# Kernel optimization log

Measured on AMD Instinct MI355X. Metric: run time of the kernel, lower is better.

Reference implementation:

```python
import jax, jax.numpy as jnp
import numpy as np

NEG_SLOPE = 0.01
H = 128  # hidden_conv_1 == hidden_conv_2


def leaky(x):
    return jnp.where(x >= 0, x, NEG_SLOPE * x)


def gru_cell(x, h, w_ih, w_hh, b_ih, b_hh):
    # PyTorch GRUCell: gates stacked [r, z, n] along dim 0 of w_ih/w_hh
    gi = x @ w_ih.T + b_ih  # [N, 3H]
    gh = h @ w_hh.T + b_hh
    ir, iz, inn = jnp.split(gi, 3, axis=-1)
    hr, hz, hn = jnp.split(gh, 3, axis=-1)
    r = jax.nn.sigmoid(ir + hr)
    z = jax.nn.sigmoid(iz + hz)
    n = jnp.tanh(inn + r * hn)
    return (1.0 - z) * n + z * h


def gcn_conv(x, w, b, src, dst, num_nodes):
    # PyG GCNConv: add self-loops, symmetric normalization, linear first
    xw = x @ w.T  # [N, H]
    loop = jnp.arange(num_nodes, dtype=src.dtype)
    s = jnp.concatenate([src, loop])
    d = jnp.concatenate([dst, loop])
    deg = jax.ops.segment_sum(jnp.ones_like(d, dtype=x.dtype), d, num_segments=num_nodes)
    dinv = jnp.where(deg > 0, jax.lax.rsqrt(deg), 0.0)
    norm = dinv[s] * dinv[d]  # [E+N]
    msg = xw[s] * norm[:, None]
    out = jax.ops.segment_sum(msg, d, num_segments=num_nodes)
    return out + b


def setup_inputs() -> dict:
    key = jax.random.key(0)
    ks = jax.random.split(key, 24)
    N, E, EL, IN_DIM, OUT_DIM = 100000, 600000, 200000, 128, 2

    def lin(k, fan_in, fan_out):
        k1, k2 = jax.random.split(k)
        bound = 1.0 / np.sqrt(fan_in)
        w = jax.random.uniform(k1, (fan_out, fan_in), minval=-bound, maxval=bound, dtype=jnp.float32)
        b = jax.random.uniform(k2, (fan_out,), minval=-bound, maxval=bound, dtype=jnp.float32)
        return w, b

    w_pre1, b_pre1 = lin(ks[0], IN_DIM, 256)
    w_pre2, b_pre2 = lin(ks[1], 256, H)
    w_c1, b_c1 = lin(ks[2], H, H)
    w_c2, b_c2 = lin(ks[3], H, H)
    w_post, b_post = lin(ks[4], H, OUT_DIM)

    def gru_params(k):
        k1, k2, k3, k4 = jax.random.split(k, 4)
        bound = 1.0 / np.sqrt(H)
        u = lambda kk, shape: jax.random.uniform(kk, shape, minval=-bound, maxval=bound, dtype=jnp.float32)
        return u(k1, (3 * H, H)), u(k2, (3 * H, H)), u(k3, (3 * H,)), u(k4, (3 * H,))

    g1_wih, g1_whh, g1_bih, g1_bhh = gru_params(ks[5])
    g2_wih, g2_whh, g2_bih, g2_bhh = gru_params(ks[6])

    x = jax.random.normal(ks[7], (N, IN_DIM), dtype=jnp.float32)
    edge_index = jax.random.randint(ks[8], (2, E), 0, N, dtype=jnp.int64 if jax.config.jax_enable_x64 else jnp.int32)
    edge_label_index = jax.random.randint(ks[9], (2, EL), 0, N, dtype=edge_index.dtype)
    prev_emb0 = jax.random.normal(ks[10], (N, H), dtype=jnp.float32)
    prev_emb1 = jax.random.normal(ks[11], (N, H), dtype=jnp.float32)

    return {
        'x': x, 'edge_index': edge_index, 'edge_label_index': edge_label_index,
        'prev_emb0': prev_emb0, 'prev_emb1': prev_emb1,
        'w_pre1': w_pre1, 'b_pre1': b_pre1, 'w_pre2': w_pre2, 'b_pre2': b_pre2,
        'w_c1': w_c1, 'b_c1': b_c1, 'w_c2': w_c2, 'b_c2': b_c2,
        'w_post': w_post, 'b_post': b_post,
        'g1_wih': g1_wih, 'g1_whh': g1_whh, 'g1_bih': g1_bih, 'g1_bhh': g1_bhh,
        'g2_wih': g2_wih, 'g2_whh': g2_whh, 'g2_bih': g2_bih, 'g2_bhh': g2_bhh,
    }


def reference(x, edge_index, edge_label_index, prev_emb0, prev_emb1,
              w_pre1, b_pre1, w_pre2, b_pre2, w_c1, b_c1, w_c2, b_c2,
              w_post, b_post, g1_wih, g1_whh, g1_bih, g1_bhh,
              g2_wih, g2_whh, g2_bih, g2_bhh):
    N = x.shape[0]
    src, dst = edge_index[0], edge_index[1]

    # preprocess (dropout p=0.0 -> identity)
    h = leaky(x @ w_pre1.T + b_pre1)
    h = leaky(h @ w_pre2.T + b_pre2)

    # unconditional GRU fuse with previous 0-hop embedding (detached in torch)
    h = jax.lax.stop_gradient(gru_cell(h, prev_emb0, g1_wih, g1_whh, g1_bih, g1_bhh))
    emb0 = h

    h = leaky(gcn_conv(h, w_c1, b_c1, src, dst, N))
    h = jax.lax.stop_gradient(gru_cell(h, prev_emb0, g1_wih, g1_whh, g1_bih, g1_bhh))
    emb1 = h

    h = leaky(gcn_conv(h, w_c2, b_c2, src, dst, N))
    h = jax.lax.stop_gradient(gru_cell(h, prev_emb1, g2_wih, g2_whh, g2_bih, g2_bhh))
    emb2 = h

    # LP head: gather + hadamard + linear + sum
    h_src = h[edge_label_index[0]]
    h_dst = h[edge_label_index[1]]
    logits = jnp.sum((h_src * h_dst) @ w_post.T + b_post, axis=-1)  # [EL]
    return logits, emb0, emb1, emb2
```

## Files before the change

### kernel.cpp

```cpp
#include <hip/hip_runtime.h>
#include <hip/hip_bf16.h>
#include <type_traits>


typedef __bf16 bf16;
typedef __bf16 bf16x8 __attribute__((ext_vector_type(8)));
typedef float  f32x4  __attribute__((ext_vector_type(4)));

#define DEV __device__ __forceinline__

DEV f32x4 mfma16(bf16x8 a, bf16x8 b, f32x4 c) {
    return __builtin_amdgcn_mfma_f32_16x16x32_bf16(a, b, c, 0, 0, 0);
}

DEV bf16x8 load_a8(const float* p) {
    f32x4 lo = *(const f32x4*)p;
    f32x4 hi = *(const f32x4*)(p + 4);
    bf16x8 v;
    v[0] = (bf16)lo[0]; v[1] = (bf16)lo[1]; v[2] = (bf16)lo[2]; v[3] = (bf16)lo[3];
    v[4] = (bf16)hi[0]; v[5] = (bf16)hi[1]; v[6] = (bf16)hi[2]; v[7] = (bf16)hi[3];
    return v;
}
DEV bf16x8 load_a8(const bf16* p) { return *(const bf16x8*)p; }

__global__ void cvt8_kernel(const float* s0, const float* s1, const float* s2, const float* s3,
                            const float* s4, const float* s5, const float* s6, const float* s7,
                            bf16* __restrict__ wb) {
    const int i = blockIdx.x * 256 + threadIdx.x;
    if (i >= 294912) return;
    float v;
    if      (i < 32768)  v = s0[i];
    else if (i < 65536)  v = s1[i - 32768];
    else if (i < 81920)  v = s2[i - 65536];
    else if (i < 98304)  v = s3[i - 81920];
    else if (i < 147456) v = s4[i - 98304];
    else if (i < 196608) v = s5[i - 147456];
    else if (i < 245760) v = s6[i - 196608];
    else                 v = s7[i - 245760];
    wb[i] = (bf16)v;
}

template<int Ci, int Co, bool ACT, bool BIAS, typename AT, typename OT>
__global__ __launch_bounds__(256) void gemm_kernel(
    const AT* __restrict__ A, const bf16* __restrict__ W,
    const float* __restrict__ bias, OT* __restrict__ C, int M)
{
    const int tid  = threadIdx.x;
    const int lane = tid & 63, w = tid >> 6;
    const int lr   = lane & 15, ko = lane >> 4;
    const int rbase = blockIdx.x * 128 + w * 32;

    constexpr int KC = Ci / 32;
    constexpr int NT = Co / 16;

    bf16x8 a[2][KC];
#pragma unroll
    for (int m = 0; m < 2; ++m) {
        long arow = rbase + m * 16 + lr; if (arow > M - 1) arow = M - 1;
#pragma unroll
        for (int kc = 0; kc < KC; ++kc)
            a[m][kc] = load_a8(A + arow * Ci + kc * 32 + ko * 8);
    }

#pragma unroll
    for (int t = 0; t < NT; ++t) {
        f32x4 acc0 = {0.f, 0.f, 0.f, 0.f};
        f32x4 acc1 = {0.f, 0.f, 0.f, 0.f};
        const bf16* wp = W + (long)(t * 16 + lr) * Ci + ko * 8;
#pragma unroll
        for (int kc = 0; kc < KC; ++kc) {
            bf16x8 wf = *(const bf16x8*)(wp + kc * 32);
            acc0 = mfma16(a[0][kc], wf, acc0);
            acc1 = mfma16(a[1][kc], wf, acc1);
        }

        const int col = t * 16 + lr;
        float bv = 0.f;
        if (BIAS) bv = bias[col];
#pragma unroll
        for (int j = 0; j < 4; ++j) {
            const int r0 = rbase + ko * 4 + j;
            if (r0 < M) {
                float v = acc0[j] + bv;
                if (ACT) v = (v >= 0.f) ? v : 0.01f * v;
                C[(long)r0 * Co + col] = (OT)v;
            }
            const int r1 = rbase + 16 + ko * 4 + j;
            if (r1 < M) {
                float v = acc1[j] + bv;
                if (ACT) v = (v >= 0.f) ? v : 0.01f * v;
                C[(long)r1 * Co + col] = (OT)v;
            }
        }
    }
}

template<typename XT>
__global__ __launch_bounds__(256) void gru_kernel(
    const XT* x, const float* __restrict__ hp,
    const bf16* __restrict__ wih, const bf16* __restrict__ whh,
    const float* __restrict__ bih, const float* __restrict__ bhh,
    float* out, int N)
{
    __shared__ bf16 Lw[6][16][128];

    const int tid  = threadIdx.x;
    const int lane = tid & 63, w = tid >> 6;
    const int lr   = lane & 15, ko = lane >> 4;
    const long rbase = (long)blockIdx.x * 64 + w * 16;

    long arow = rbase + lr; if (arow > N - 1) arow = N - 1;
    bf16x8 ax[4], ah[4];
#pragma unroll
    for (int kc = 0; kc < 4; ++kc) {
        ax[kc] = load_a8(x  + arow * 128 + kc * 32 + ko * 8);
        ah[kc] = load_a8(hp + arow * 128 + kc * 32 + ko * 8);
    }

    bf16x8 pre[6];
    auto LDW = [&](int tc) {
#pragma unroll
        for (int i = 0; i < 6; ++i) {
            const int ch  = tid + 256 * i;
            const int g   = ch >> 8, rem = ch & 255;
            const int row = rem >> 4, cc = rem & 15;
            const int scc = cc ^ (row & 7);
            pre[i] = *(const bf16x8*)((g < 3 ? wih : whh)
                + (long)(((g % 3) * 128 + tc * 16 + row) * 128 + scc * 8));
        }
    };
    LDW(0);

    for (int tc = 0; tc < 8; ++tc) {
        __syncthreads();
#pragma unroll
        for (int i = 0; i < 6; ++i) {
            const int ch  = tid + 256 * i;
            const int g   = ch >> 8, rem = ch & 255;
            const int row = rem >> 4, cc = rem & 15;
            *(bf16x8*)(&Lw[g][row][cc * 8]) = pre[i];
        }
        __syncthreads();
        if (tc < 7) LDW(tc + 1);

        const int col = tc * 16 + lr;
        const float br = bih[col]       + bhh[col];
        const float bz = bih[128 + col] + bhh[128 + col];
        const float bi = bih[256 + col];
        const float bh = bhh[256 + col];

        f32x4 ar = {0.f, 0.f, 0.f, 0.f};
        f32x4 az = {0.f, 0.f, 0.f, 0.f};
        f32x4 ai = {0.f, 0.f, 0.f, 0.f};
        f32x4 ag = {0.f, 0.f, 0.f, 0.f};
#pragma unroll
        for (int kc = 0; kc < 4; ++kc) {
            const int cc = (kc * 4 + ko) ^ (lr & 7);
            bf16x8 wr_i = *(const bf16x8*)(&Lw[0][lr][cc * 8]);
            bf16x8 wz_i = *(const bf16x8*)(&Lw[1][lr][cc * 8]);
            bf16x8 wn_i = *(const bf16x8*)(&Lw[2][lr][cc * 8]);
            bf16x8 wr_h = *(const bf16x8*)(&Lw[3][lr][cc * 8]);
            bf16x8 wz_h = *(const bf16x8*)(&Lw[4][lr][cc * 8]);
            bf16x8 wn_h = *(const bf16x8*)(&Lw[5][lr][cc * 8]);
            ar = mfma16(ax[kc], wr_i, ar);
            ar = mfma16(ah[kc], wr_h, ar);
            az = mfma16(ax[kc], wz_i, az);
            az = mfma16(ah[kc], wz_h, az);
            ai = mfma16(ax[kc], wn_i, ai);
            ag = mfma16(ah[kc], wn_h, ag);
        }
#pragma unroll
        for (int j = 0; j < 4; ++j) {
            const long row = rbase + ko * 4 + j;
            if (row < N) {
                const float r = 1.f / (1.f + __expf(-(ar[j] + br)));
                const float z = 1.f / (1.f + __expf(-(az[j] + bz)));
                const float pre_ = (ai[j] + bi) + r * (ag[j] + bh);
                const float n = 1.f - 2.f / (1.f + __expf(2.f * pre_));
                out[row * 128 + col] = (1.f - z) * n + z * hp[row * 128 + col];
            }
        }
    }
}

__global__ void deg_kernel(const int* __restrict__ dst, int* degi, int E) {
    const int e = blockIdx.x * 256 + threadIdx.x;
    if (e < E) atomicAdd(&degi[dst[e]], 1);
}

__global__ void scan1_kernel(const int* __restrict__ degi, int* __restrict__ inc,
                             int* __restrict__ bsum, float* __restrict__ dinv, int N) {
    __shared__ int s[256];
    const int i = blockIdx.x * 256 + threadIdx.x;
    const int d = (i < N) ? degi[i] : 0;
    if (i < N) dinv[i] = rsqrtf((float)d + 1.0f);
    s[threadIdx.x] = d;
    __syncthreads();
#pragma unroll
    for (int off = 1; off < 256; off <<= 1) {
        int t = (threadIdx.x >= off) ? s[threadIdx.x - off] : 0;
        __syncthreads();
        s[threadIdx.x] += t;
        __syncthreads();
    }
    if (i < N) inc[i] = s[threadIdx.x];
    if (threadIdx.x == 255) bsum[blockIdx.x] = s[255];
}

__global__ void scan2_kernel(int* bsum, int nb) {
    __shared__ int s[512];
    __shared__ int carry;
    if (threadIdx.x == 0) carry = 0;
    __syncthreads();
    for (int base = 0; base < nb; base += 512) {
        const int i = base + threadIdx.x;
        s[threadIdx.x] = (i < nb) ? bsum[i] : 0;
        __syncthreads();
#pragma unroll
        for (int off = 1; off < 512; off <<= 1) {
            int t = (threadIdx.x >= off) ? s[threadIdx.x - off] : 0;
            __syncthreads();
            s[threadIdx.x] += t;
            __syncthreads();
        }
        const int c = carry;
        if (i < nb) bsum[i] = s[threadIdx.x] + c;
        __syncthreads();
        if (threadIdx.x == 511) carry = c + s[511];
        __syncthreads();
    }
}

__global__ void scan3_kernel(const int* __restrict__ inc, const int* __restrict__ degi,
                             const int* __restrict__ bsum, int* __restrict__ rowptr,
                             int* __restrict__ rp2, int N) {
    const int i = blockIdx.x * 256 + threadIdx.x;
    if (i >= N) return;
    const int prev = (blockIdx.x > 0) ? bsum[blockIdx.x - 1] : 0;
    const int rp = prev + inc[i] - degi[i];
    rowptr[i] = rp;
    rp2[i]    = rp;
}

__global__ void fill_kernel(const int* __restrict__ src, const int* __restrict__ dst,
                            int* rp2, const float* __restrict__ dinv,
                            int* __restrict__ csr_src, float* __restrict__ csr_norm, int E) {
    const int e = blockIdx.x * 256 + threadIdx.x;
    if (e >= E) return;
    const int s = src[e], d = dst[e];
    const int pos = atomicAdd(&rp2[d], 1);
    csr_src[pos]  = s;
    csr_norm[pos] = dinv[s] * dinv[d];
}

template<typename OT>
__global__ __launch_bounds__(256) void gather_kernel(
    const bf16* __restrict__ xwb,
    const int* __restrict__ rowptr, const int* __restrict__ degi,
    const int* __restrict__ csr_src, const float* __restrict__ csr_norm,
    const float* __restrict__ dinv, const float* __restrict__ bias,
    OT* __restrict__ out, int N, int colbase, int cw, int lg)
{
    const long tid = (long)blockIdx.x * 256 + threadIdx.x;
    const long d = tid >> lg;
    const int  c = (int)(tid & ((1 << lg) - 1));
    if (d >= N) return;

    const int start = rowptr[d];
    const int deg   = degi[d];
    const int h     = deg >> 1;
    const bf16* xb  = xwb + c * 8;

    float acca[8] = {0.f, 0.f, 0.f, 0.f, 0.f, 0.f, 0.f, 0.f};
    float accb[8] = {0.f, 0.f, 0.f, 0.f, 0.f, 0.f, 0.f, 0.f};
    for (int k = 0; k < h; ++k) {
        const int   sa = csr_src[start + k];
        const int   sb = csr_src[start + h + k];
        const float na = csr_norm[start + k];
        const float nb_ = csr_norm[start + h + k];
        bf16x8 va = *(const bf16x8*)(xb + (long)sa * cw);
        bf16x8 vb = *(const bf16x8*)(xb + (long)sb * cw);
#pragma unroll
        for (int j = 0; j < 8; ++j) {
            acca[j] += (float)va[j] * na;
            accb[j] += (float)vb[j] * nb_;
        }
    }
    if (deg & 1) {
        const int   s  = csr_src[start + deg - 1];
        const float nm = csr_norm[start + deg - 1];
        bf16x8 v = *(const bf16x8*)(xb + (long)s * cw);
#pragma unroll
        for (int j = 0; j < 8; ++j) acca[j] += (float)v[j] * nm;
    }

    const float di = dinv[d], sl = di * di;
    bf16x8 vd = *(const bf16x8*)(xb + d * cw);
    const int col = colbase + c * 8;
    float v[8];
#pragma unroll
    for (int j = 0; j < 8; ++j) {
        float t = acca[j] + accb[j] + (float)vd[j] * sl + bias[col + j];
        v[j] = (t >= 0.f) ? t : 0.01f * t;
    }
    if constexpr (std::is_same<OT, bf16>::value) {
        bf16x8 o;
#pragma unroll
        for (int j = 0; j < 8; ++j) o[j] = (bf16)v[j];
        *(bf16x8*)(out + d * 128 + col) = o;
    } else {
        f32x4 o0, o1;
#pragma unroll
        for (int j = 0; j < 4; ++j) { o0[j] = v[j]; o1[j] = v[4 + j]; }
        *(f32x4*)(out + d * 128 + col)     = o0;
        *(f32x4*)(out + d * 128 + col + 4) = o1;
    }
}

__global__ __launch_bounds__(256) void lp_kernel(
    const float* __restrict__ emb, const int* __restrict__ eli,
    const float* __restrict__ wpost, const float* __restrict__ bpost,
    float* __restrict__ logits, int EL)
{
    const int e = blockIdx.x * 256 + threadIdx.x;
    if (e >= EL) return;
    const long s = eli[e], d = eli[EL + e];
    float acc = 0.f;
#pragma unroll
    for (int c = 0; c < 32; ++c) {
        f32x4 vs = *(const f32x4*)(emb + s * 128 + c * 4);
        f32x4 vd = *(const f32x4*)(emb + d * 128 + c * 4);
        f32x4 w0 = *(const f32x4*)(wpost + c * 4);
        f32x4 w1 = *(const f32x4*)(wpost + 128 + c * 4);
#pragma unroll
        for (int i = 0; i < 4; ++i)
            acc += vs[i] * vd[i] * (w0[i] + w1[i]);
    }
    logits[e] = acc + bpost[0] + bpost[1];
}

extern "C" void kernel_launch(void* const* d_in, const int* in_sizes, int n_in,
                              void* d_out, int out_size, void* d_ws, size_t ws_size,
                              hipStream_t stream) {
    const float* x      = (const float*)d_in[0];
    const int*   ei     = (const int*)d_in[1];
    const int*   eli    = (const int*)d_in[2];
    const float* prev0  = (const float*)d_in[3];
    const float* prev1  = (const float*)d_in[4];
    const float* w_pre1 = (const float*)d_in[5];
    const float* b_pre1 = (const float*)d_in[6];
    const float* w_pre2 = (const float*)d_in[7];
    const float* b_pre2 = (const float*)d_in[8];
    const float* w_c1   = (const float*)d_in[9];
    const float* b_c1   = (const float*)d_in[10];
    const float* w_c2   = (const float*)d_in[11];
    const float* b_c2   = (const float*)d_in[12];
    const float* w_post = (const float*)d_in[13];
    const float* b_post = (const float*)d_in[14];
    const float* g1_wih = (const float*)d_in[15];
    const float* g1_whh = (const float*)d_in[16];
    const float* g1_bih = (const float*)d_in[17];
    const float* g1_bhh = (const float*)d_in[18];
    const float* g2_wih = (const float*)d_in[19];
    const float* g2_whh = (const float*)d_in[20];
    const float* g2_bih = (const float*)d_in[21];
    const float* g2_bhh = (const float*)d_in[22];

    const int N  = in_sizes[0] / 128;
    const int E  = in_sizes[1] / 2;
    const int EL = in_sizes[2] / 2;
    const long NH = (long)N * 128;

    float* out    = (float*)d_out;
    float* logits = out;
    float* emb0   = out + EL;
    float* emb1   = emb0 + NH;
    float* emb2   = emb1 + NH;

    bf16* H1b = (bf16*)emb1;
    bf16* H2b = (bf16*)emb2;
    bf16* h1b = (bf16*)emb2;

    char* ws = (char*)d_ws;
    size_t p = 0;
    auto alloc = [&](size_t bytes) { size_t o = p; p = (p + bytes + 255) & ~(size_t)255; return o; };
    float* dinv    = (float*)(ws + alloc((size_t)N * 4));
    int*   degi    = (int*)  (ws + alloc((size_t)N * 4));
    int*   inc     = (int*)  (ws + alloc((size_t)N * 4));
    int*   rowptr  = (int*)  (ws + alloc((size_t)N * 4));
    int*   rp2     = (int*)  (ws + alloc((size_t)N * 4));
    int*   bsum    = (int*)  (ws + alloc(4096));
    bf16*  wb      = (bf16*) (ws + alloc((size_t)294912 * 2));
    int*   csr_src = (int*)  (ws + alloc((size_t)E * 4));
    float* csr_nrm = (float*)(ws + alloc((size_t)E * 4));
    const size_t fixed = p;
    bf16*  xwb     = (bf16*)(ws + fixed);

    int cw = 128;
    while (cw > 16 && fixed + (size_t)N * cw * 2 > ws_size) cw >>= 1;
    const int lg = __builtin_ctz(cw >> 3);
    const int passes = 128 / cw;

    const bool big_ws = (cw == 128) &&
        (ws_size >= fixed + (size_t)N * 128 * 2 + (size_t)N * 128 * 2);
    bf16* h2b = big_ws ? (bf16*)(ws + fixed + (size_t)N * 128 * 2) : nullptr;

    bf16* wb_pre1 = wb;
    bf16* wb_pre2 = wb_pre1 + 32768;
    bf16* wb_c1   = wb_pre2 + 32768;
    bf16* wb_c2   = wb_c1 + 16384;
    bf16* wb_g1i  = wb_c2 + 16384;
    bf16* wb_g1h  = wb_g1i + 49152;
    bf16* wb_g2i  = wb_g1h + 49152;
    bf16* wb_g2h  = wb_g2i + 49152;

    const int gB = 256;
    const dim3 blk(gB);
    const int grid_rows128 = (N + 127) / 128;
    const int grid_gru     = (N + 63) / 64;
    const int grid_E       = (E + gB - 1) / gB;
    const int nb           = (N + 255) / 256;

    cvt8_kernel<<<(294912 + 255) / 256, blk, 0, stream>>>(
        w_pre1, w_pre2, w_c1, w_c2, g1_wih, g1_whh, g2_wih, g2_whh, wb);

    hipMemsetAsync(degi, 0, (size_t)N * 4, stream);
    deg_kernel<<<grid_E, blk, 0, stream>>>(ei + E, degi, E);
    scan1_kernel<<<nb, blk, 0, stream>>>(degi, inc, bsum, dinv, N);
    scan2_kernel<<<1, 512, 0, stream>>>(bsum, nb);
    scan3_kernel<<<nb, blk, 0, stream>>>(inc, degi, bsum, rowptr, rp2, N);
    fill_kernel<<<grid_E, blk, 0, stream>>>(ei, ei + E, rp2, dinv, csr_src, csr_nrm, E);

    gemm_kernel<128, 256, true, true, float, bf16><<<grid_rows128, blk, 0, stream>>>(x, wb_pre1, b_pre1, H1b, N);
    gemm_kernel<256, 128, true, true, bf16,  bf16><<<grid_rows128, blk, 0, stream>>>(H1b, wb_pre2, b_pre2, H2b, N);

    gru_kernel<bf16><<<grid_gru, blk, 0, stream>>>(H2b, prev0, wb_g1i, wb_g1h, g1_bih, g1_bhh, emb0, N);

    const int grid_ga = (int)((((long)N << lg) + gB - 1) / gB);
    auto run_gemm = [&](const float* hin, const bf16* wp) {
        switch (cw) {
        case 128: gemm_kernel<128, 128, false, false, float, bf16><<<grid_rows128, blk, 0, stream>>>(hin, wp, nullptr, xwb, N); break;
        case 64:  gemm_kernel<128, 64,  false, false, float, bf16><<<grid_rows128, blk, 0, stream>>>(hin, wp, nullptr, xwb, N); break;
        case 32:  gemm_kernel<128, 32,  false, false, float, bf16><<<grid_rows128, blk, 0, stream>>>(hin, wp, nullptr, xwb, N); break;
        default:  gemm_kernel<128, 16,  false, false, float, bf16><<<grid_rows128, blk, 0, stream>>>(hin, wp, nullptr, xwb, N); break;
        }
    };

    for (int ps = 0; ps < passes; ++ps) {
        run_gemm(emb0, wb_c1 + (size_t)(ps * cw) * 128);
        gather_kernel<bf16><<<grid_ga, blk, 0, stream>>>(xwb, rowptr, degi, csr_src, csr_nrm,
                                                         dinv, b_c1, h1b, N, ps * cw, cw, lg);
    }
    gru_kernel<bf16><<<grid_gru, blk, 0, stream>>>(h1b, prev0, wb_g1i, wb_g1h, g1_bih, g1_bhh, emb1, N);

    for (int ps = 0; ps < passes; ++ps) {
        run_gemm(emb1, wb_c2 + (size_t)(ps * cw) * 128);
        if (big_ws)
            gather_kernel<bf16><<<grid_ga, blk, 0, stream>>>(xwb, rowptr, degi, csr_src, csr_nrm,
                                                             dinv, b_c2, h2b, N, ps * cw, cw, lg);
        else
            gather_kernel<float><<<grid_ga, blk, 0, stream>>>(xwb, rowptr, degi, csr_src, csr_nrm,
                                                              dinv, b_c2, emb2, N, ps * cw, cw, lg);
    }
    if (big_ws)
        gru_kernel<bf16><<<grid_gru, blk, 0, stream>>>(h2b, prev1, wb_g2i, wb_g2h, g2_bih, g2_bhh, emb2, N);
    else
        gru_kernel<float><<<grid_gru, blk, 0, stream>>>(emb2, prev1, wb_g2i, wb_g2h, g2_bih, g2_bhh, emb2, N);

    lp_kernel<<<(EL + gB - 1) / gB, blk, 0, stream>>>(emb2, eli, w_post, b_post, logits, EL);
}
```

Before: 545.4 us.

## Fuse GCN gather into GRU, cooperative CSR build, and widen LP head

Adds a gg_kernel that performs the GCN neighbor aggregation, self-loop, bias and leaky ReLU in registers and feeds them straight into the GRU MFMA, removing the intermediate h1b/h2b round trip and separate gather launches. The five CSR-construction launches plus memset are replaced by a single cooperative kernel with grid-wide syncs, with the old path kept as a fallback if the cooperative launch fails. The LP head now uses 16 threads per edge with a shuffle reduction instead of one thread per edge. The risk is that the fused kernel does the irregular per-row gather with one lane-row per thread, which can diverge badly and lower occupancy, and the cooperative grid of 1024 blocks serialises phases.

Result: slower. 1.074 ms (+96.9%).

```diff
diff --git a/kernel.cpp b/kernel.cpp
--- a/kernel.cpp
+++ b/kernel.cpp
@@ -1,6 +1,9 @@
 #include <hip/hip_runtime.h>
 #include <hip/hip_bf16.h>
+#include <hip/hip_cooperative_groups.h>
 #include <type_traits>
+
+namespace cg = cooperative_groups;
 
 
 typedef __bf16 bf16;
@@ -183,11 +186,210 @@
     }
 }
 
+__global__ __launch_bounds__(256) void gg_kernel(
+    const bf16* __restrict__ xwb,
+    const int* __restrict__ rowptr, const int* __restrict__ degi,
+    const int* __restrict__ csr_src, const float* __restrict__ csr_norm,
+    const float* __restrict__ dinv, const float* __restrict__ cbias,
+    const float* __restrict__ hp,
+    const bf16* __restrict__ wih, const bf16* __restrict__ whh,
+    const float* __restrict__ bih, const float* __restrict__ bhh,
+    float* __restrict__ out, int N)
+{
+    __shared__ bf16 Lw[6][16][128];
+
+    const int tid  = threadIdx.x;
+    const int lane = tid & 63, w = tid >> 6;
+    const int lr   = lane & 15, ko = lane >> 4;
+    const long rbase = (long)blockIdx.x * 64 + w * 16;
+
+    long arow = rbase + lr; if (arow > N - 1) arow = N - 1;
+
+    float acc[4][8];
+#pragma unroll
+    for (int kc = 0; kc < 4; ++kc)
+#pragma unroll
+        for (int j = 0; j < 8; ++j) acc[kc][j] = 0.f;
+    {
+        const int start = rowptr[arow];
+        const int deg   = degi[arow];
+        const bf16* xb  = xwb + ko * 8;
+        for (int k = 0; k < deg; ++k) {
+            const int   s  = csr_src[start + k];
+            const float nm = csr_norm[start + k];
+            const bf16* vp = xb + (long)s * 128;
+            bf16x8 v0 = *(const bf16x8*)(vp);
+            bf16x8 v1 = *(const bf16x8*)(vp + 32);
+            bf16x8 v2 = *(const bf16x8*)(vp + 64);
+            bf16x8 v3 = *(const bf16x8*)(vp + 96);
+#pragma unroll
+            for (int j = 0; j < 8; ++j) {
+                acc[0][j] += (float)v0[j] * nm;
+                acc[1][j] += (float)v1[j] * nm;
+                acc[2][j] += (float)v2[j] * nm;
+                acc[3][j] += (float)v3[j] * nm;
+            }
+        }
+    }
+
+    bf16x8 ax[4], ah[4];
+    {
+        const float di = dinv[arow], sl = di * di;
+        const bf16* vp = xwb + (long)arow * 128 + ko * 8;
+#pragma unroll
+        for (int kc = 0; kc < 4; ++kc) {
+            bf16x8 vd = *(const bf16x8*)(vp + kc * 32);
+#pragma unroll
+            for (int j = 0; j < 8; ++j) {
+                float t = acc[kc][j] + (float)vd[j] * sl + cbias[kc * 32 + ko * 8 + j];
+                t = (t >= 0.f) ? t : 0.01f * t;
+                ax[kc][j] = (bf16)t;
+            }
+            ah[kc] = load_a8(hp + arow * 128 + kc * 32 + ko * 8);
+        }
+    }
+
+    bf16x8 pre[6];
+    auto LDW = [&](int tc) {
+#pragma unroll
+        for (int i = 0; i < 6; ++i) {
+            const int ch  = tid + 256 * i;
+            const int g   = ch >> 8, rem = ch & 255;
+            const int row = rem >> 4, cc = rem & 15;
+            const int scc = cc ^ (row & 7);
+            pre[i] = *(const bf16x8*)((g < 3 ? wih : whh)
+                + (long)(((g % 3) * 128 + tc * 16 + row) * 128 + scc * 8));
+        }
+    };
+    LDW(0);
+
+    for (int tc = 0; tc < 8; ++tc) {
+        __syncthreads();
+#pragma unroll
+        for (int i = 0; i < 6; ++i) {
+            const int ch  = tid + 256 * i;
+            const int g   = ch >> 8, rem = ch & 255;
+            const int row = rem >> 4, cc = rem & 15;
+            *(bf16x8*)(&Lw[g][row][cc * 8]) = pre[i];
+        }
+        __syncthreads();
+        if (tc < 7) LDW(tc + 1);
+
+        const int col = tc * 16 + lr;
+        const float br = bih[col]       + bhh[col];
+        const float bz = bih[128 + col] + bhh[128 + col];
+        const float bi = bih[256 + col];
+        const float bh = bhh[256 + col];
+
+        f32x4 ar = {0.f, 0.f, 0.f, 0.f};
+        f32x4 az = {0.f, 0.f, 0.f, 0.f};
+        f32x4 ai = {0.f, 0.f, 0.f, 0.f};
+        f32x4 ag = {0.f, 0.f, 0.f, 0.f};
+#pragma unroll
+        for (int kc = 0; kc < 4; ++kc) {
+            const int cc = (kc * 4 + ko) ^ (lr & 7);
+            bf16x8 wr_i = *(const bf16x8*)(&Lw[0][lr][cc * 8]);
+            bf16x8 wz_i = *(const bf16x8*)(&Lw[1][lr][cc * 8]);
+            bf16x8 wn_i = *(const bf16x8*)(&Lw[2][lr][cc * 8]);
+            bf16x8 wr_h = *(const bf16x8*)(&Lw[3][lr][cc * 8]);
+            bf16x8 wz_h = *(const bf16x8*)(&Lw[4][lr][cc * 8]);
+            bf16x8 wn_h = *(const bf16x8*)(&Lw[5][lr][cc * 8]);
+            ar = mfma16(ax[kc], wr_i, ar);
+            ar = mfma16(ah[kc], wr_h, ar);
+            az = mfma16(ax[kc], wz_i, az);
+            az = mfma16(ah[kc], wz_h, az);
+            ai = mfma16(ax[kc], wn_i, ai);
+            ag = mfma16(ah[kc], wn_h, ag);
+        }
+#pragma unroll
+        for (int j = 0; j < 4; ++j) {
+            const long row = rbase + ko * 4 + j;
+            if (row < N) {
+                const float r = 1.f / (1.f + __expf(-(ar[j] + br)));
+                const float z = 1.f / (1.f + __expf(-(az[j] + bz)));
+                const float pre_ = (ai[j] + bi) + r * (ag[j] + bh);
+                const float n = 1.f - 2.f / (1.f + __expf(2.f * pre_));
+                out[row * 128 + col] = (1.f - z) * n + z * hp[row * 128 + col];
+            }
+        }
+    }
+}
+
+__global__ void csr_coop_kernel(const int* __restrict__ src, const int* __restrict__ dst,
+                                int* degi, float* dinv, int* inc, int* bsum,
+                                int* rowptr, int* rp2,
+                                int* csr_src, float* csr_nrm, int N, int E, int nb)
+{
+    cg::grid_group grid = cg::this_grid();
+    __shared__ int s[256];
+    __shared__ int carry;
+    const int gsz  = gridDim.x * 256;
+    const int gtid = blockIdx.x * 256 + threadIdx.x;
+
+    for (int i = gtid; i < N; i += gsz) degi[i] = 0;
+    grid.sync();
+    for (int e = gtid; e < E; e += gsz) atomicAdd(&degi[dst[e]], 1);
+    grid.sync();
+    for (int c = blockIdx.x; c < nb; c += gridDim.x) {
+        const int i = c * 256 + threadIdx.x;
+        const int d = (i < N) ? degi[i] : 0;
+        if (i < N) dinv[i] = rsqrtf((float)d + 1.0f);
+        s[threadIdx.x] = d;
+        __syncthreads();
+#pragma unroll
+        for (int off = 1; off < 256; off <<= 1) {
+            int t = (threadIdx.x >= off) ? s[threadIdx.x - off] : 0;
+            __syncthreads();
+            s[threadIdx.x] += t;
+            __syncthreads();
+        }
+        if (i < N) inc[i] = s[threadIdx.x];
+        if (threadIdx.x == 255) bsum[c] = s[255];
+        __syncthreads();
+    }
+    grid.sync();
+    if (blockIdx.x == 0) {
+        if (threadIdx.x == 0) carry = 0;
+        __syncthreads();
+        for (int base = 0; base < nb; base += 256) {
+            const int i = base + threadIdx.x;
+            s[threadIdx.x] = (i < nb) ? bsum[i] : 0;
+            __syncthreads();
+#pragma unroll
+            for (int off = 1; off < 256; off <<= 1) {
+                int t = (threadIdx.x >= off) ? s[threadIdx.x - off] : 0;
+                __syncthreads();
+                s[threadIdx.x] += t;
+                __syncthreads();
+            }
+            const int cy = carry;
+            if (i < nb) bsum[i] = s[threadIdx.x] + cy;
+            __syncthreads();
+            if (threadIdx.x == 255) carry = cy + s[255];
+            __syncthreads();
+        }
+    }
+    grid.sync();
+    for (int i = gtid; i < N; i += gsz) {
+        const int c = i >> 8;
+        const int prev = (c > 0) ? bsum[c - 1] : 0;
+        const int rp = prev + inc[i] - degi[i];
+        rowptr[i] = rp;
+        rp2[i]    = rp;
+    }
+    grid.sync();
+    for (int e = gtid; e < E; e += gsz) {
+        const int sv = src[e], d = dst[e];
+        const int pos = atomicAdd(&rp2[d], 1);
+        csr_src[pos] = sv;
+        csr_nrm[pos] = dinv[sv] * dinv[d];
+    }
+}
+
 __global__ void deg_kernel(const int* __restrict__ dst, int* degi, int E) {
     const int e = blockIdx.x * 256 + threadIdx.x;
     if (e < E) atomicAdd(&degi[dst[e]], 1);
 }
-
 __global__ void scan1_kernel(const int* __restrict__ degi, int* __restrict__ inc,
                              int* __restrict__ bsum, float* __restrict__ dinv, int N) {
     __shared__ int s[256];
@@ -206,7 +408,6 @@
     if (i < N) inc[i] = s[threadIdx.x];
     if (threadIdx.x == 255) bsum[blockIdx.x] = s[255];
 }
-
 __global__ void scan2_kernel(int* bsum, int nb) {
     __shared__ int s[512];
     __shared__ int carry;
@@ -230,7 +431,6 @@
         __syncthreads();
     }
 }
-
 __global__ void scan3_kernel(const int* __restrict__ inc, const int* __restrict__ degi,
                              const int* __restrict__ bsum, int* __restrict__ rowptr,
                              int* __restrict__ rp2, int N) {
@@ -241,7 +441,6 @@
     rowptr[i] = rp;
     rp2[i]    = rp;
 }
-
 __global__ void fill_kernel(const int* __restrict__ src, const int* __restrict__ dst,
                             int* rp2, const float* __restrict__ dinv,
                             int* __restrict__ csr_src, float* __restrict__ csr_norm, int E) {
@@ -322,21 +521,30 @@
     const float* __restrict__ wpost, const float* __restrict__ bpost,
     float* __restrict__ logits, int EL)
 {
-    const int e = blockIdx.x * 256 + threadIdx.x;
+    const long t = (long)blockIdx.x * 256 + threadIdx.x;
+    const long e = t >> 4;
+    const int  c = (int)(t & 15);
     if (e >= EL) return;
     const long s = eli[e], d = eli[EL + e];
+
+    f32x4 a0 = *(const f32x4*)(emb + s * 128 + c * 8);
+    f32x4 a1 = *(const f32x4*)(emb + s * 128 + c * 8 + 4);
+    f32x4 b0 = *(const f32x4*)(emb + d * 128 + c * 8);
+    f32x4 b1 = *(const f32x4*)(emb + d * 128 + c * 8 + 4);
+    f32x4 w00 = *(const f32x4*)(wpost + c * 8);
+    f32x4 w01 = *(const f32x4*)(wpost + c * 8 + 4);
+    f32x4 w10 = *(const f32x4*)(wpost + 128 + c * 8);
+    f32x4 w11 = *(const f32x4*)(wpost + 128 + c * 8 + 4);
+
     float acc = 0.f;
 #pragma unroll
-    for (int c = 0; c < 32; ++c) {
-        f32x4 vs = *(const f32x4*)(emb + s * 128 + c * 4);
-        f32x4 vd = *(const f32x4*)(emb + d * 128 + c * 4);
-        f32x4 w0 = *(const f32x4*)(wpost + c * 4);
-        f32x4 w1 = *(const f32x4*)(wpost + 128 + c * 4);
-#pragma unroll
-        for (int i = 0; i < 4; ++i)
-            acc += vs[i] * vd[i] * (w0[i] + w1[i]);
-    }
-    logits[e] = acc + bpost[0] + bpost[1];
+    for (int i = 0; i < 4; ++i) {
+        acc += a0[i] * b0[i] * (w00[i] + w10[i]);
+        acc += a1[i] * b1[i] * (w01[i] + w11[i]);
+    }
+#pragma unroll
+    for (int m = 1; m < 16; m <<= 1) acc += __shfl_xor(acc, m);
+    if (c == 0) logits[e] = acc + bpost[0] + bpost[1];
 }
 
 extern "C" void kernel_launch(void* const* d_in, const int* in_sizes, int n_in,
@@ -400,8 +608,8 @@
     while (cw > 16 && fixed + (size_t)N * cw * 2 > ws_size) cw >>= 1;
     const int lg = __builtin_ctz(cw >> 3);
     const int passes = 128 / cw;
-
-    const bool big_ws = (cw == 128) &&
+    const bool fused = (cw == 128);
+    const bool big_ws = fused &&
         (ws_size >= fixed + (size_t)N * 128 * 2 + (size_t)N * 128 * 2);
     bf16* h2b = big_ws ? (bf16*)(ws + fixed + (size_t)N * 128 * 2) : nullptr;
 
@@ -424,19 +632,31 @@
     cvt8_kernel<<<(294912 + 255) / 256, blk, 0, stream>>>(
         w_pre1, w_pre2, w_c1, w_c2, g1_wih, g1_whh, g2_wih, g2_whh, wb);
 
-    hipMemsetAsync(degi, 0, (size_t)N * 4, stream);
-    deg_kernel<<<grid_E, blk, 0, stream>>>(ei + E, degi, E);
-    scan1_kernel<<<nb, blk, 0, stream>>>(degi, inc, bsum, dinv, N);
-    scan2_kernel<<<1, 512, 0, stream>>>(bsum, nb);
-    scan3_kernel<<<nb, blk, 0, stream>>>(inc, degi, bsum, rowptr, rp2, N);
-    fill_kernel<<<grid_E, blk, 0, stream>>>(ei, ei + E, rp2, dinv, csr_src, csr_nrm, E);
+    {
+        const int* srcp = ei;
+        const int* dstp = ei + E;
+        int N_ = N, E_ = E, nb_ = nb;
+        void* args[] = { (void*)&srcp, (void*)&dstp, (void*)&degi, (void*)&dinv,
+                         (void*)&inc, (void*)&bsum, (void*)&rowptr, (void*)&rp2,
+                         (void*)&csr_src, (void*)&csr_nrm,
+                         (void*)&N_, (void*)&E_, (void*)&nb_ };
+        hipError_t err = hipLaunchCooperativeKernel(
+            reinterpret_cast<void*>(&csr_coop_kernel), dim3(1024), dim3(256), args, 0, stream);
+        if (err != hipSuccess) {
+            hipMemsetAsync(degi, 0, (size_t)N * 4, stream);
+            deg_kernel<<<grid_E, blk, 0, stream>>>(ei + E, degi, E);
+            scan1_kernel<<<nb, blk, 0, stream>>>(degi, inc, bsum, dinv, N);
+            scan2_kernel<<<1, 512, 0, stream>>>(bsum, nb);
+            scan3_kernel<<<nb, blk, 0, stream>>>(inc, degi, bsum, rowptr, rp2, N);
+            fill_kernel<<<grid_E, blk, 0, stream>>>(ei, ei + E, rp2, dinv, csr_src, csr_nrm, E);
+        }
+    }
 
     gemm_kernel<128, 256, true, true, float, bf16><<<grid_rows128, blk, 0, stream>>>(x, wb_pre1, b_pre1, H1b, N);
     gemm_kernel<256, 128, true, true, bf16,  bf16><<<grid_rows128, blk, 0, stream>>>(H1b, wb_pre2, b_pre2, H2b, N);
 
     gru_kernel<bf16><<<grid_gru, blk, 0, stream>>>(H2b, prev0, wb_g1i, wb_g1h, g1_bih, g1_bhh, emb0, N);
 
-    const int grid_ga = (int)((((long)N << lg) + gB - 1) / gB);
     auto run_gemm = [&](const float* hin, const bf16* wp) {
         switch (cw) {
         case 128: gemm_kernel<128, 128, false, false, float, bf16><<<grid_rows128, blk, 0, stream>>>(hin, wp, nullptr, xwb, N); break;
@@ -446,26 +666,37 @@
         }
     };
 
-    for (int ps = 0; ps < passes; ++ps) {
-        run_gemm(emb0, wb_c1 + (size_t)(ps * cw) * 128);
-        gather_kernel<bf16><<<grid_ga, blk, 0, stream>>>(xwb, rowptr, degi, csr_src, csr_nrm,
-                                                         dinv, b_c1, h1b, N, ps * cw, cw, lg);
-    }
-    gru_kernel<bf16><<<grid_gru, blk, 0, stream>>>(h1b, prev0, wb_g1i, wb_g1h, g1_bih, g1_bhh, emb1, N);
-
-    for (int ps = 0; ps < passes; ++ps) {
-        run_gemm(emb1, wb_c2 + (size_t)(ps * cw) * 128);
+    if (fused) {
+        run_gemm(emb0, wb_c1);
+        gg_kernel<<<grid_gru, blk, 0, stream>>>(xwb, rowptr, degi, csr_src, csr_nrm,
+                                                dinv, b_c1, prev0,
+                                                wb_g1i, wb_g1h, g1_bih, g1_bhh, emb1, N);
+        run_gemm(emb1, wb_c2);
+        gg_kernel<<<grid_gru, blk, 0, stream>>>(xwb, rowptr, degi, csr_src, csr_nrm,
+                                                dinv, b_c2, prev1,
+                                                wb_g2i, wb_g2h, g2_bih, g2_bhh, emb2, N);
+    } else {
+        const int grid_ga = (int)((((long)N << lg) + gB - 1) / gB);
+        for (int ps = 0; ps < passes; ++ps) {
+            run_gemm(emb0, wb_c1 + (size_t)(ps * cw) * 128);
+            gather_kernel<bf16><<<grid_ga, blk, 0, stream>>>(xwb, rowptr, degi, csr_src, csr_nrm,
+                                                             dinv, b_c1, h1b, N, ps * cw, cw, lg);
+        }
+        gru_kernel<bf16><<<grid_gru, blk, 0, stream>>>(h1b, prev0, wb_g1i, wb_g1h, g1_bih, g1_bhh, emb1, N);
+        for (int ps = 0; ps < passes; ++ps) {
+            run_gemm(emb1, wb_c2 + (size_t)(ps * cw) * 128);
+            if (big_ws)
+                gather_kernel<bf16><<<grid_ga, blk, 0, stream>>>(xwb, rowptr, degi, csr_src, csr_nrm,
+                                                                 dinv, b_c2, h2b, N, ps * cw, cw, lg);
+            else
+                gather_kernel<float><<<grid_ga, blk, 0, stream>>>(xwb, rowptr, degi, csr_src, csr_nrm,
+                                                                  dinv, b_c2, emb2, N, ps * cw, cw, lg);
+        }
         if (big_ws)
-            gather_kernel<bf16><<<grid_ga, blk, 0, stream>>>(xwb, rowptr, degi, csr_src, csr_nrm,
-                                                             dinv, b_c2, h2b, N, ps * cw, cw, lg);
+            gru_kernel<bf16><<<grid_gru, blk, 0, stream>>>(h2b, prev1, wb_g2i, wb_g2h, g2_bih, g2_bhh, emb2, N);
         else
-            gather_kernel<float><<<grid_ga, blk, 0, stream>>>(xwb, rowptr, degi, csr_src, csr_nrm,
-                                                              dinv, b_c2, emb2, N, ps * cw, cw, lg);
-    }
-    if (big_ws)
-        gru_kernel<bf16><<<grid_gru, blk, 0, stream>>>(h2b, prev1, wb_g2i, wb_g2h, g2_bih, g2_bhh, emb2, N);
-    else
-        gru_kernel<float><<<grid_gru, blk, 0, stream>>>(emb2, prev1, wb_g2i, wb_g2h, g2_bih, g2_bhh, emb2, N);
-
-    lp_kernel<<<(EL + gB - 1) / gB, blk, 0, stream>>>(emb2, eli, w_post, b_post, logits, EL);
-}
+            gru_kernel<float><<<grid_gru, blk, 0, stream>>>(emb2, prev1, wb_g2i, wb_g2h, g2_bih, g2_bhh, emb2, N);
+    }
+
+    lp_kernel<<<(int)(((long)EL * 16 + gB - 1) / gB), blk, 0, stream>>>(emb2, eli, w_post, b_post, logits, EL);
+}
```
